# Kernel optimization log

Measured on AMD Instinct MI355X. Metric: run time of the kernel, lower is better.

## Reference

```python
import jax, jax.numpy as jnp
import numpy as np

N = 256
M = 180


def _fft3_centered(u):
    # centered 3D FFT: shift so that frequency 0 is at index n//2
    return jnp.fft.fftshift(jnp.fft.fftn(jnp.fft.ifftshift(u)))


def _ifft2_centered(s):
    ax = (-2, -1)
    return jnp.fft.fftshift(jnp.fft.ifft2(jnp.fft.ifftshift(s, axes=ax), axes=ax), axes=ax)


def _trilinear(F, pos):
    """Sample complex 3D grid F (n,n,n) at fractional index positions pos (...,3).
    Points outside the grid contribute zero (frequencies beyond Nyquist)."""
    n = F.shape[0]
    p0f = jnp.floor(pos)
    f = pos - p0f                      # fractional part, in [0,1)
    p0 = p0f.astype(jnp.int32)
    acc = jnp.zeros(pos.shape[:-1], dtype=F.dtype)
    for dx in (0, 1):
        for dy in (0, 1):
            for dz in (0, 1):
                idx = p0 + jnp.array([dx, dy, dz], jnp.int32)
                w = ((f[..., 0] if dx else 1.0 - f[..., 0])
                     * (f[..., 1] if dy else 1.0 - f[..., 1])
                     * (f[..., 2] if dz else 1.0 - f[..., 2]))
                valid = jnp.all((idx >= 0) & (idx < n), axis=-1)
                idc = jnp.clip(idx, 0, n - 1)
                val = F[idc[..., 0], idc[..., 1], idc[..., 2]]  # irregular gather
                acc = acc + jnp.where(valid, w, 0.0) * val
    return acc


def _lamino_fwd(weight, theta, tilt):
    """NUFFT laminography forward projector (Fourier-slice formulation).
    weight: (n,n,n,2) real/imag volume; theta: (M,) angles; tilt: scalar.
    Returns (M,n,n,2) projections, matching tike's Lamino.fwd math: the 2D
    Fourier transform of each projection equals the 3D FT of the volume
    sampled on a plane tilted by `tilt` and rotated by `theta` about z."""
    n = weight.shape[0]
    u = jax.lax.complex(weight[..., 0], weight[..., 1])
    F = _fft3_centered(u)                                   # (n,n,n) complex64
    fr = ((jnp.arange(n) - n // 2) / n).astype(jnp.float32)  # [-0.5, 0.5)
    kv, ku = jnp.meshgrid(fr, fr, indexing='ij')            # detector freq grid
    ct, st = jnp.cos(theta), jnp.sin(theta)                 # (M,)
    cp_, sp = jnp.cos(tilt), jnp.sin(tilt)
    one = jnp.ones_like(ct)
    e_u = jnp.stack([ct, st, 0.0 * ct], -1)                 # (M,3) horizontal axis
    e_v = jnp.stack([-st * cp_, ct * cp_, sp * one], -1)    # (M,3) tilted axis
    # 3D non-uniform frequencies for every (angle, detector pixel): (M,n,n,3)
    k3 = ku[None, :, :, None] * e_u[:, None, None, :] + kv[None, :, :, None] * e_v[:, None, None, :]
    pos = k3 * n + n // 2                                   # fractional grid coords
    samples = _trilinear(F, pos)                            # (M,n,n) complex
    proj = _ifft2_centered(samples)                         # (M,n,n) complex
    return jnp.stack([proj.real, proj.imag], -1).astype(jnp.float32)


def setup_inputs() -> dict:
    key = jax.random.key(0)
    k1, k2 = jax.random.split(key)
    weight = jax.random.normal(k1, (N, N, N, 2), dtype=jnp.float32)
    theta = jax.random.uniform(k2, (M,), dtype=jnp.float32) * (2.0 * np.pi)
    tilt = jnp.float32(1.0)  # laminography tilt angle (rad); source default pi/2
    return {"weight": weight, "theta": theta, "tilt": tilt}


def reference(weight, theta, tilt):
    return _lamino_fwd(weight, theta, tilt)
```

## Files before the change

### kernel.cpp

```cpp
#include <hip/hip_runtime.h>
#include <math.h>


namespace {

template<int MODE, bool INV>
__global__ __launch_bounds__(256)
void fft_pass(const float2* in, float2* out) {
  __shared__ float sre[8][265];
  __shared__ float sim[8][265];
  __shared__ float twr[128];
  __shared__ float twi[128];
  const int t = threadIdx.x;
  if (t < 128) {
    const float TWO_PI = 6.28318530717958647692f;
    float ang = (INV ? TWO_PI : -TWO_PI) * ((float)t * (1.0f / 256.0f));
    float s, c;
    sincosf(ang, &s, &c);
    twr[t] = c;
    twi[t] = s;
  }
  int l, j0, base, stride;
  if (MODE == 0) { l = t >> 5; j0 = t & 31; }
  else           { l = t & 7;  j0 = t >> 3; }
  const int lineIdx = (int)blockIdx.x * 8 + l;
  if (MODE == 0)      { base = lineIdx * 256;                            stride = 1;     }
  else if (MODE == 1) { base = (lineIdx >> 8) * 65536 + (lineIdx & 255); stride = 256;   }
  else                { base = lineIdx;                                  stride = 65536; }

  #pragma unroll
  for (int r = 0; r < 8; r++) {
    int j = j0 + 32 * r;
    float2 v = in[base + j * stride];
    float sgn = (j & 1) ? -1.0f : 1.0f;
    sre[l][j] = v.x * sgn;
    sim[l][j] = v.y * sgn;
  }
  __syncthreads();

  const int line = t >> 5;
  const int lane = t & 31;
  #pragma unroll
  for (int s = 0; s < 8; s++) {
    const int half = 128 >> s;
    #pragma unroll
    for (int r = 0; r < 4; r++) {
      int b   = lane + 32 * r;
      int pos = b & (half - 1);
      int grp = b >> (7 - s);
      int i   = (grp << (8 - s)) + pos;
      int j   = i + half;
      float ar = sre[line][i], ai = sim[line][i];
      float br = sre[line][j], bi = sim[line][j];
      sre[line][i] = ar + br;
      sim[line][i] = ai + bi;
      float dr = ar - br, di = ai - bi;
      int mm = pos << s;
      float wr = twr[mm], wi = twi[mm];
      sre[line][j] = dr * wr - di * wi;
      sim[line][j] = dr * wi + di * wr;
    }
    __syncthreads();
  }

  const float scale = INV ? (1.0f / 256.0f) : 1.0f;
  #pragma unroll
  for (int r = 0; r < 8; r++) {
    int j = j0 + 32 * r;
    int rev = (int)(__brev((unsigned)j) >> 24);
    float sgn = (j & 1) ? -scale : scale;
    float2 v;
    v.x = sre[l][rev] * sgn;
    v.y = sim[l][rev] * sgn;
    out[base + j * stride] = v;
  }
}

__global__ __launch_bounds__(256)
void sample_kernel(const float2* __restrict__ F, float2* __restrict__ out,
                   const float* __restrict__ theta, const float* __restrict__ tiltp) {
  const int m = blockIdx.z;
  const int b = blockIdx.x * 16 + threadIdx.x;
  const int a = blockIdx.y * 16 + threadIdx.y;
  float th = theta[m];
  float ct = cosf(th), st = sinf(th);
  float tl = tiltp[0];
  float cp = cosf(tl), sp = sinf(tl);
  float bu = (float)(b - 128);
  float av = (float)(a - 128);
  float p0 = bu * ct + av * (-st * cp) + 128.0f;
  float p1 = bu * st + av * (ct * cp) + 128.0f;
  float p2 = av * sp + 128.0f;
  float f0 = floorf(p0), f1 = floorf(p1), f2 = floorf(p2);
  int x0 = (int)f0, y0 = (int)f1, z0 = (int)f2;
  float fx = p0 - f0, fy = p1 - f1, fz = p2 - f2;
  float accr = 0.0f, acci = 0.0f;
  #pragma unroll
  for (int dx = 0; dx < 2; dx++) {
    int x = x0 + dx;
    bool vx = (x >= 0) && (x < 256);
    int xc = min(max(x, 0), 255);
    float wx = dx ? fx : (1.0f - fx);
    #pragma unroll
    for (int dy = 0; dy < 2; dy++) {
      int y = y0 + dy;
      bool vy = vx && (y >= 0) && (y < 256);
      int yc = min(max(y, 0), 255);
      float wxy = wx * (dy ? fy : (1.0f - fy));
      int rowbase = (xc * 256 + yc) * 256;
      #pragma unroll
      for (int dz = 0; dz < 2; dz++) {
        int z = z0 + dz;
        bool v = vy && (z >= 0) && (z < 256);
        int zc = min(max(z, 0), 255);
        float w = v ? wxy * (dz ? fz : (1.0f - fz)) : 0.0f;
        float2 c = F[rowbase + zc];
        accr += w * c.x;
        acci += w * c.y;
      }
    }
  }
  out[(m * 256 + a) * 256 + b] = make_float2(accr, acci);
}

}

extern "C" void kernel_launch(void* const* d_in, const int* in_sizes, int n_in,
                              void* d_out, int out_size, void* d_ws, size_t ws_size,
                              hipStream_t stream) {
  const float2* w  = (const float2*)d_in[0];
  const float*  th = (const float*)d_in[1];
  const float*  tl = (const float*)d_in[2];
  float2* F    = (float2*)d_ws;
  float2* out2 = (float2*)d_out;

  fft_pass<0, false><<<8192, 256, 0, stream>>>(w, F);
  fft_pass<1, false><<<8192, 256, 0, stream>>>(F, F);
  fft_pass<2, false><<<8192, 256, 0, stream>>>(F, F);

  dim3 g(16, 16, 180), blk(16, 16);
  sample_kernel<<<g, blk, 0, stream>>>(F, out2, th, tl);

  fft_pass<0, true><<<5760, 256, 0, stream>>>(out2, out2);
  fft_pass<1, true><<<5760, 256, 0, stream>>>(out2, out2);
}
```

Before: 647.3 us.

## Widen strided FFT passes to 16 lines with float4 loads; retile sampling kernel

Splits the FFT pass into a contiguous-row kernel and a strided kernel. The strided kernel handles 16 lines per block and loads and stores two adjacent complex values per float4, so each row segment fetched along the strided axis is 128 bytes rather than 64. The sampling kernel switches to 32x8 blocks with four output rows per thread, which widens each warp's row of outputs and amortises the per-angle trig setup. The cost is more LDS per block and more work per thread, which may lower occupancy.

```diff
diff --git a/kernel.cpp b/kernel.cpp
--- a/kernel.cpp
+++ b/kernel.cpp
@@ -4,9 +4,9 @@
 
 namespace {
 
-template<int MODE, bool INV>
+template<bool INV>
 __global__ __launch_bounds__(256)
-void fft_pass(const float2* in, float2* out) {
+void fft_contig(const float2* in, float2* out) {
   __shared__ float sre[8][265];
   __shared__ float sim[8][265];
   __shared__ float twr[128];
@@ -15,31 +15,23 @@
   if (t < 128) {
     const float TWO_PI = 6.28318530717958647692f;
     float ang = (INV ? TWO_PI : -TWO_PI) * ((float)t * (1.0f / 256.0f));
-    float s, c;
-    sincosf(ang, &s, &c);
-    twr[t] = c;
-    twi[t] = s;
-  }
-  int l, j0, base, stride;
-  if (MODE == 0) { l = t >> 5; j0 = t & 31; }
-  else           { l = t & 7;  j0 = t >> 3; }
-  const int lineIdx = (int)blockIdx.x * 8 + l;
-  if (MODE == 0)      { base = lineIdx * 256;                            stride = 1;     }
-  else if (MODE == 1) { base = (lineIdx >> 8) * 65536 + (lineIdx & 255); stride = 256;   }
-  else                { base = lineIdx;                                  stride = 65536; }
-
-  #pragma unroll
-  for (int r = 0; r < 8; r++) {
-    int j = j0 + 32 * r;
-    float2 v = in[base + j * stride];
+    float s, c; sincosf(ang, &s, &c);
+    twr[t] = c; twi[t] = s;
+  }
+  const int l = t >> 5, j0 = t & 31;
+  const int base = ((int)blockIdx.x * 8 + l) * 256;
+
+  #pragma unroll
+  for (int r = 0; r < 8; r++) {
+    int j = j0 + 32 * r;
+    float2 v = in[base + j];
     float sgn = (j & 1) ? -1.0f : 1.0f;
     sre[l][j] = v.x * sgn;
     sim[l][j] = v.y * sgn;
   }
   __syncthreads();
 
-  const int line = t >> 5;
-  const int lane = t & 31;
+  const int line = t >> 5, lane = t & 31;
   #pragma unroll
   for (int s = 0; s < 8; s++) {
     const int half = 128 >> s;
@@ -72,7 +64,81 @@
     float2 v;
     v.x = sre[l][rev] * sgn;
     v.y = sim[l][rev] * sgn;
-    out[base + j * stride] = v;
+    out[base + j] = v;
+  }
+}
+
+template<int MODE, bool INV>
+__global__ __launch_bounds__(256)
+void fft_strided(const float2* in, float2* out) {
+  __shared__ float sre[16][266];
+  __shared__ float sim[16][266];
+  __shared__ float twr[128];
+  __shared__ float twi[128];
+  const int t = threadIdx.x;
+  if (t < 128) {
+    const float TWO_PI = 6.28318530717958647692f;
+    float ang = (INV ? TWO_PI : -TWO_PI) * ((float)t * (1.0f / 256.0f));
+    float s, c; sincosf(ang, &s, &c);
+    twr[t] = c; twi[t] = s;
+  }
+  const int lp = (t & 7) * 2;
+  const int j0 = t >> 3;
+  const int lineIdx0 = (int)blockIdx.x * 16;
+  int base, stride;
+  if (MODE == 1) { base = (lineIdx0 >> 8) * 65536 + (lineIdx0 & 255); stride = 256;   }
+  else           { base = lineIdx0;                                   stride = 65536; }
+  const float4* in4  = (const float4*)in;
+  float4*       out4 = (float4*)out;
+
+  #pragma unroll
+  for (int r = 0; r < 8; r++) {
+    int j = j0 + 32 * r;
+    float4 v = in4[(base + j * stride + lp) >> 1];
+    float sgn = (j & 1) ? -1.0f : 1.0f;
+    sre[lp][j]     = v.x * sgn;
+    sim[lp][j]     = v.y * sgn;
+    sre[lp + 1][j] = v.z * sgn;
+    sim[lp + 1][j] = v.w * sgn;
+  }
+  __syncthreads();
+
+  const int line = t >> 4, lane = t & 15;
+  #pragma unroll
+  for (int s = 0; s < 8; s++) {
+    const int half = 128 >> s;
+    #pragma unroll
+    for (int r = 0; r < 8; r++) {
+      int b   = lane + 16 * r;
+      int pos = b & (half - 1);
+      int grp = b >> (7 - s);
+      int i   = (grp << (8 - s)) + pos;
+      int j   = i + half;
+      float ar = sre[line][i], ai = sim[line][i];
+      float br = sre[line][j], bi = sim[line][j];
+      sre[line][i] = ar + br;
+      sim[line][i] = ai + bi;
+      float dr = ar - br, di = ai - bi;
+      int mm = pos << s;
+      float wr = twr[mm], wi = twi[mm];
+      sre[line][j] = dr * wr - di * wi;
+      sim[line][j] = dr * wi + di * wr;
+    }
+    __syncthreads();
+  }
+
+  const float scale = INV ? (1.0f / 256.0f) : 1.0f;
+  #pragma unroll
+  for (int r = 0; r < 8; r++) {
+    int j = j0 + 32 * r;
+    int rev = (int)(__brev((unsigned)j) >> 24);
+    float sgn = (j & 1) ? -scale : scale;
+    float4 v;
+    v.x = sre[lp][rev]     * sgn;
+    v.y = sim[lp][rev]     * sgn;
+    v.z = sre[lp + 1][rev] * sgn;
+    v.w = sim[lp + 1][rev] * sgn;
+    out4[(base + j * stride + lp) >> 1] = v;
   }
 }
 
@@ -80,47 +146,54 @@
 void sample_kernel(const float2* __restrict__ F, float2* __restrict__ out,
                    const float* __restrict__ theta, const float* __restrict__ tiltp) {
   const int m = blockIdx.z;
-  const int b = blockIdx.x * 16 + threadIdx.x;
-  const int a = blockIdx.y * 16 + threadIdx.y;
+  const int b = blockIdx.x * 32 + threadIdx.x;
+  const int a0 = blockIdx.y * 32 + threadIdx.y;
   float th = theta[m];
   float ct = cosf(th), st = sinf(th);
   float tl = tiltp[0];
   float cp = cosf(tl), sp = sinf(tl);
-  float bu = (float)(b - 128);
-  float av = (float)(a - 128);
-  float p0 = bu * ct + av * (-st * cp) + 128.0f;
-  float p1 = bu * st + av * (ct * cp) + 128.0f;
-  float p2 = av * sp + 128.0f;
-  float f0 = floorf(p0), f1 = floorf(p1), f2 = floorf(p2);
-  int x0 = (int)f0, y0 = (int)f1, z0 = (int)f2;
-  float fx = p0 - f0, fy = p1 - f1, fz = p2 - f2;
-  float accr = 0.0f, acci = 0.0f;
-  #pragma unroll
-  for (int dx = 0; dx < 2; dx++) {
-    int x = x0 + dx;
-    bool vx = (x >= 0) && (x < 256);
-    int xc = min(max(x, 0), 255);
-    float wx = dx ? fx : (1.0f - fx);
+  const float eu0 = ct, eu1 = st;
+  const float ev0 = -st * cp, ev1 = ct * cp, ev2 = sp;
+  const float bu = (float)(b - 128);
+
+  #pragma unroll
+  for (int k = 0; k < 4; k++) {
+    const int a = a0 + 8 * k;
+    const float av = (float)(a - 128);
+    float p0 = bu * eu0 + av * ev0 + 128.0f;
+    float p1 = bu * eu1 + av * ev1 + 128.0f;
+    float p2 = av * ev2 + 128.0f;
+    float f0 = floorf(p0), f1 = floorf(p1), f2 = floorf(p2);
+    int x0 = (int)f0, y0 = (int)f1, z0 = (int)f2;
+    float fx = p0 - f0, fy = p1 - f1, fz = p2 - f2;
+    float accr = 0.0f, acci = 0.0f;
     #pragma unroll
-    for (int dy = 0; dy < 2; dy++) {
-      int y = y0 + dy;
-      bool vy = vx && (y >= 0) && (y < 256);
-      int yc = min(max(y, 0), 255);
-      float wxy = wx * (dy ? fy : (1.0f - fy));
-      int rowbase = (xc * 256 + yc) * 256;
+    for (int dx = 0; dx < 2; dx++) {
+      int x = x0 + dx;
+      bool vx = (x >= 0) && (x < 256);
+      int xc = min(max(x, 0), 255);
+      float wx = dx ? fx : (1.0f - fx);
       #pragma unroll
-      for (int dz = 0; dz < 2; dz++) {
-        int z = z0 + dz;
-        bool v = vy && (z >= 0) && (z < 256);
-        int zc = min(max(z, 0), 255);
-        float w = v ? wxy * (dz ? fz : (1.0f - fz)) : 0.0f;
-        float2 c = F[rowbase + zc];
-        accr += w * c.x;
-        acci += w * c.y;
+      for (int dy = 0; dy < 2; dy++) {
+        int y = y0 + dy;
+        bool vy = vx && (y >= 0) && (y < 256);
+        int yc = min(max(y, 0), 255);
+        float wxy = wx * (dy ? fy : (1.0f - fy));
+        int rowbase = (xc * 256 + yc) * 256;
+        #pragma unroll
+        for (int dz = 0; dz < 2; dz++) {
+          int z = z0 + dz;
+          bool v = vy && (z >= 0) && (z < 256);
+          int zc = min(max(z, 0), 255);
+          float w = v ? wxy * (dz ? fz : (1.0f - fz)) : 0.0f;
+          float2 c = F[rowbase + zc];
+          accr += w * c.x;
+          acci += w * c.y;
+        }
       }
     }
-  }
-  out[(m * 256 + a) * 256 + b] = make_float2(accr, acci);
+    out[(m * 256 + a) * 256 + b] = make_float2(accr, acci);
+  }
 }
 
 }
@@ -134,13 +207,13 @@
   float2* F    = (float2*)d_ws;
   float2* out2 = (float2*)d_out;
 
-  fft_pass<0, false><<<8192, 256, 0, stream>>>(w, F);
-  fft_pass<1, false><<<8192, 256, 0, stream>>>(F, F);
-  fft_pass<2, false><<<8192, 256, 0, stream>>>(F, F);
-
-  dim3 g(16, 16, 180), blk(16, 16);
+  fft_contig<false><<<8192, 256, 0, stream>>>(w, F);
+  fft_strided<1, false><<<4096, 256, 0, stream>>>(F, F);
+  fft_strided<2, false><<<4096, 256, 0, stream>>>(F, F);
+
+  dim3 g(8, 8, 180), blk(32, 8);
   sample_kernel<<<g, blk, 0, stream>>>(F, out2, th, tl);
 
-  fft_pass<0, true><<<5760, 256, 0, stream>>>(out2, out2);
-  fft_pass<1, true><<<5760, 256, 0, stream>>>(out2, out2);
-}
+  fft_contig<true><<<5760, 256, 0, stream>>>(out2, out2);
+  fft_strided<1, true><<<2880, 256, 0, stream>>>(out2, out2);
+}
```

After: 711.8 us. +10.0%, slower.
